# Performance work log

Hardware: AMD Instinct MI355X
Metric: run time of the kernel (lower is better)

Reference implementation:

```python
import math
import jax, jax.numpy as jnp
import numpy as np

NUM_HEADS = 8
ATTN_STD = np.array([1.0, 2.0, 4.0, 8.0, 1.0, 2.0, 4.0, 8.0], dtype=np.float32)
ATTN_OFFSET = np.array([-1.0, -2.0, -4.0, -8.0, -1.0, -2.0, -4.0, -8.0], dtype=np.float32)


def setup_inputs() -> dict:
    key = jax.random.key(0)
    k1, k2, k3 = jax.random.split(key, 3)
    B, L, D = 2, 2048, 1024
    values = jax.random.normal(k1, (B, L, D), dtype=jnp.float32)
    # learned params (init_std = 0.02, matching nn.init.normal_)
    input_weights = 0.02 * jax.random.normal(k2, (D, D), dtype=jnp.float32)
    output_weight = 0.02 * jax.random.normal(k3, (D, D), dtype=jnp.float32)
    return {"values": values, "input_weights": input_weights, "output_weight": output_weight}


def _gaussian_attn_weights(qlen, dtype):
    # Faithful closed form of get_attn_cache retrieval for offsets <= -1:
    # w[h, q, k] = N(k - q - offset_h; std_h), no renormalization, no mask.
    stds = jnp.asarray(ATTN_STD, dtype=dtype)[:, None, None]      # [H,1,1]
    offs = jnp.asarray(ATTN_OFFSET, dtype=dtype)[:, None, None]   # [H,1,1]
    q = jnp.arange(qlen, dtype=dtype)[None, :, None]               # [1,L,1]
    k = jnp.arange(qlen, dtype=dtype)[None, None, :]               # [1,1,L]
    dist = k - q - offs                                            # [H,L,L]
    inv_norm = 1.0 / (stds * math.sqrt(2.0 * math.pi))
    return inv_norm * jnp.exp(-0.5 * (dist / stds) ** 2)           # [H,L,L]


def reference(values, input_weights, output_weight):
    B, L, D = values.shape
    H = NUM_HEADS
    pd = D // H
    # project(): F.linear(values, input_weights) then split into heads
    v = values @ input_weights.T                                   # [B,L,D]
    v = v.reshape(B, L, H, pd).transpose(0, 2, 1, 3)               # [B,H,L,pd]
    probs = _gaussian_attn_weights(L, values.dtype)                # [H,L,L]
    attended = jnp.einsum('hqk,bhkd->bhqd', probs, v)              # [B,H,L,pd]
    attended = attended.transpose(0, 2, 1, 3).reshape(B, L, D)     # merge heads
    # output_projection (Linear, no bias)
    return attended @ output_weight.T
```

## Files before the change

kernel.cpp:

```cpp
#include <hip/hip_runtime.h>
#include <hip/hip_bf16.h>

#define L_SEQ   2048
#define D_MODEL 1024
#define B_SZ    2
#define LP      (L_SEQ + 192)
#define PADF    96

typedef __attribute__((ext_vector_type(8))) short bf16x8;
typedef __attribute__((ext_vector_type(4))) float f32x4;

__device__ __forceinline__ void gll16(const void* g, void* l) {
    __builtin_amdgcn_global_load_lds(
        (const __attribute__((address_space(1))) unsigned int*)(g),
        (__attribute__((address_space(3))) unsigned int*)(l),
        16, 0, 0);
}

__device__ __forceinline__ ushort bf16_hi(float x) {
    __hip_bfloat16 h = __float2bfloat16(x);
    return *reinterpret_cast<ushort*>(&h);
}
__device__ __forceinline__ float bf16_back(ushort u) {
    __hip_bfloat16 h = *reinterpret_cast<__hip_bfloat16*>(&u);
    return __bfloat162float(h);
}

__global__ __launch_bounds__(256) void prep(const float* __restrict__ values,
                                            const float* __restrict__ w_in,
                                            const float* __restrict__ w_out,
                                            ushort* __restrict__ Ph, ushort* __restrict__ Pl,
                                            ushort* __restrict__ Wh, ushort* __restrict__ Wl,
                                            ushort* __restrict__ W2h, ushort* __restrict__ W2l,
                                            float* __restrict__ vpad)
{
    int blk = blockIdx.x;
    if (blk < 384) {
        const int r  = blk / 96;
        const int rr = blk % 96;
        const int b  = r >> 1;
        const int row0 = (r & 1) ? (LP - 96) : 0;
        size_t off = ((size_t)b * LP + row0 + rr) * D_MODEL + threadIdx.x * 4;
        *(float4*)(vpad + off) = make_float4(0.f, 0.f, 0.f, 0.f);
        return;
    }
    blk -= 384;
    const float* src;
    ushort *oh, *ol;
    if (blk < 4096)      { src = values; oh = Ph;  ol = Pl;  }
    else if (blk < 5120) { src = w_in;   oh = Wh;  ol = Wl;  blk -= 4096; }
    else                 { src = w_out;  oh = W2h; ol = W2l; blk -= 5120; }

    const size_t i = ((size_t)blk * 256 + threadIdx.x) * 4;
    float4 v = *(const float4*)(src + i);
    float f[4] = {v.x, v.y, v.z, v.w};
    ushort hb[4], lb[4];
    #pragma unroll
    for (int j = 0; j < 4; ++j) {
        hb[j] = bf16_hi(f[j]);
        lb[j] = bf16_hi(f[j] - bf16_back(hb[j]));
    }
    *(ushort4*)(oh + i) = make_ushort4(hb[0], hb[1], hb[2], hb[3]);
    *(ushort4*)(ol + i) = make_ushort4(lb[0], lb[1], lb[2], lb[3]);
}

template<int DO_PAD>
__global__ __launch_bounds__(512) void gemm_split(const ushort* __restrict__ Ah,
                                                  const ushort* __restrict__ Al,
                                                  const ushort* __restrict__ Bh,
                                                  const ushort* __restrict__ Bl,
                                                  float* __restrict__ C)
{
    __shared__ __align__(16) ushort lds[4][4][128 * 32];

    const int tid = threadIdx.x;
    const int w   = tid >> 6;
    const int l   = tid & 63;

    const int bn  = (blockIdx.x & 7) * 128;
    const int bm  = (blockIdx.x >> 3) * 128;

    const int srow   = tid >> 2;
    const int schunk = (tid & 3) ^ ((tid >> 3) & 3);
    const ushort* gAh = Ah + (size_t)(bm + srow) * 1024 + schunk * 8;
    const ushort* gAl = Al + (size_t)(bm + srow) * 1024 + schunk * 8;
    const ushort* gBh = Bh + (size_t)(bn + srow) * 1024 + schunk * 8;
    const ushort* gBl = Bl + (size_t)(bn + srow) * 1024 + schunk * 8;
    const int ldst = tid * 8;

    const int fr  = l & 15;
    const int fq  = l >> 4;
    const int swz = (fr >> 1) & 3;
    const int rdo = (fq ^ swz) << 3;
    const int wr  = w >> 2;
    const int wc  = w & 3;

    f32x4 acc[4][2];
    #pragma unroll
    for (int mi = 0; mi < 4; ++mi)
        #pragma unroll
        for (int ni = 0; ni < 2; ++ni) acc[mi][ni] = (f32x4){0.f, 0.f, 0.f, 0.f};

    #define STAGE(buf, kt)                                        \
        do {                                                      \
            const size_t ko_ = (size_t)(kt) * 32;                 \
            gll16(gAh + ko_, &lds[(buf)][0][ldst]);               \
            gll16(gAl + ko_, &lds[(buf)][1][ldst]);               \
            gll16(gBh + ko_, &lds[(buf)][2][ldst]);               \
            gll16(gBl + ko_, &lds[(buf)][3][ldst]);               \
        } while (0)

    #define WAITBAR(N) asm volatile("s_waitcnt vmcnt(" #N ")\n\ts_barrier" ::: "memory")

    #define COMPUTE(cur)                                                                   \
        do {                                                                               \
            bf16x8 ah[4], al[4];                                                           \
            _Pragma("unroll")                                                              \
            for (int mi = 0; mi < 4; ++mi) {                                               \
                const int row = wr * 64 + mi * 16 + fr;                                    \
                ah[mi] = *(const bf16x8*)&lds[(cur)][0][row * 32 + rdo];                   \
                al[mi] = *(const bf16x8*)&lds[(cur)][1][row * 32 + rdo];                   \
            }                                                                              \
            _Pragma("unroll")                                                              \
            for (int ni = 0; ni < 2; ++ni) {                                               \
                const int row = wc * 32 + ni * 16 + fr;                                    \
                bf16x8 bh = *(const bf16x8*)&lds[(cur)][2][row * 32 + rdo];                \
                bf16x8 bl = *(const bf16x8*)&lds[(cur)][3][row * 32 + rdo];                \
                _Pragma("unroll")                                                          \
                for (int mi = 0; mi < 4; ++mi)                                             \
                    acc[mi][ni] = __builtin_amdgcn_mfma_f32_16x16x32_bf16(ah[mi], bh, acc[mi][ni], 0, 0, 0); \
                _Pragma("unroll")                                                          \
                for (int mi = 0; mi < 4; ++mi)                                             \
                    acc[mi][ni] = __builtin_amdgcn_mfma_f32_16x16x32_bf16(al[mi], bh, acc[mi][ni], 0, 0, 0); \
                _Pragma("unroll")                                                          \
                for (int mi = 0; mi < 4; ++mi)                                             \
                    acc[mi][ni] = __builtin_amdgcn_mfma_f32_16x16x32_bf16(ah[mi], bl, acc[mi][ni], 0, 0, 0); \
            }                                                                              \
        } while (0)

    STAGE(0, 0);
    STAGE(1, 1);
    STAGE(2, 2);

    for (int kt = 0; kt < 29; ++kt) {
        WAITBAR(8);
        STAGE((kt + 3) & 3, kt + 3);
        COMPUTE(kt & 3);
    }
    WAITBAR(8); COMPUTE(1);
    WAITBAR(4); COMPUTE(2);
    WAITBAR(0); COMPUTE(3);

    #undef STAGE
    #undef WAITBAR
    #undef COMPUTE

    #pragma unroll
    for (int mi = 0; mi < 4; ++mi) {
        #pragma unroll
        for (int ni = 0; ni < 2; ++ni) {
            const int col = bn + wc * 32 + ni * 16 + fr;
            #pragma unroll
            for (int j = 0; j < 4; ++j) {
                const int m = bm + wr * 64 + mi * 16 + fq * 4 + j;
                const size_t row = DO_PAD ? ((size_t)(m >> 11) * LP + (m & (L_SEQ - 1)) + PADF)
                                          : (size_t)m;
                C[row * 1024 + col] = acc[mi][ni][j];
            }
        }
    }
}

__global__ __launch_bounds__(256) void gauss_conv_split(const float* __restrict__ vpad,
                                                        ushort* __restrict__ Oh,
                                                        ushort* __restrict__ Ol)
{
    __shared__ __align__(16) float xs[256 * 64];
    __shared__ float wt[128];

    const int tid = threadIdx.x;
    const int d0  = blockIdx.x * 64;
    const int q0  = blockIdx.y * 128;
    const int b   = blockIdx.z;
    const int h   = blockIdx.x >> 1;

    if (tid < 128) {
        const float sig = (float)(1 << (h & 3));
        const float t = ((float)(tid - 71) + sig) / sig;
        wt[tid] = (0.39894228040143267794f / sig) * expf(-0.5f * t * t);
    }

    const float* src = vpad + ((size_t)b * LP + (PADF - 71) + q0) * 1024 + d0;
    #pragma unroll
    for (int p = 0; p < 16; ++p) {
        const int f   = p * 256 + tid;
        const int row = f >> 4;
        const int c4  = (f & 15) * 4;
        gll16(src + (size_t)row * 1024 + c4, &xs[f * 4]);
    }
    __syncthreads();

    const int d     = tid & 63;
    const int qbase = (tid >> 6) * 32;

    float acc[32];
    #pragma unroll
    for (int qq = 0; qq < 32; ++qq) acc[qq] = 0.f;

    #pragma unroll 1
    for (int c = 0; c < 8; ++c) {
        float xw[47];
        const float* xp = &xs[(qbase + c * 16) * 64 + d];
        #pragma unroll
        for (int j = 0; j < 47; ++j) xw[j] = xp[j * 64];
        #pragma unroll
        for (int dd = 0; dd < 16; ++dd) {
            const float wv = wt[c * 16 + dd];
            #pragma unroll
            for (int qq = 0; qq < 32; ++qq)
                acc[qq] = fmaf(wv, xw[dd + qq], acc[qq]);
        }
    }

    ushort* oh = Oh + ((size_t)b * L_SEQ + q0 + qbase) * 1024 + d0 + d;
    ushort* ol = Ol + ((size_t)b * L_SEQ + q0 + qbase) * 1024 + d0 + d;
    #pragma unroll
    for (int qq = 0; qq < 32; ++qq) {
        const ushort hv = bf16_hi(acc[qq]);
        oh[(size_t)qq * 1024] = hv;
        ol[(size_t)qq * 1024] = bf16_hi(acc[qq] - bf16_back(hv));
    }
}

extern "C" void kernel_launch(void* const* d_in, const int* in_sizes, int n_in,
                              void* d_out, int out_size, void* d_ws, size_t ws_size,
                              hipStream_t stream)
{
    const float* values = (const float*)d_in[0];
    const float* w_in   = (const float*)d_in[1];
    const float* w_out  = (const float*)d_in[2];
    float* out = (float*)d_out;

    float*  vpad = (float*)d_ws;
    ushort* Ph  = (ushort*)(vpad + (size_t)B_SZ * LP * D_MODEL);
    ushort* Pl  = Ph  + (size_t)4096 * 1024;
    ushort* Wh  = Pl  + (size_t)4096 * 1024;
    ushort* Wl  = Wh  + (size_t)1024 * 1024;
    ushort* W2h = Wl  + (size_t)1024 * 1024;
    ushort* W2l = W2h + (size_t)1024 * 1024;

    prep<<<dim3(384 + 4096 + 1024 + 1024), dim3(256), 0, stream>>>(
        values, w_in, w_out, Ph, Pl, Wh, Wl, W2h, W2l, vpad);

    gemm_split<1><<<dim3(256), dim3(512), 0, stream>>>(Ph, Pl, Wh, Wl, vpad);

    dim3 cgrid(D_MODEL / 64, L_SEQ / 128, B_SZ);
    gauss_conv_split<<<cgrid, dim3(256), 0, stream>>>(vpad, Ph, Pl);

    gemm_split<0><<<dim3(256), dim3(512), 0, stream>>>(Ph, Pl, W2h, W2l, out);
}
```

Before: 151.2 us.

## Split GEMM into 128x64 tiles with 256 threads, triple-buffered LDS, XCD-aware mapping

The split-bf16 GEMM now uses 128x64 output tiles computed by 4 waves, so 512 blocks launch instead of 256 and two blocks can share a CU. The LDS pipeline drops from four stages to three, which shrinks shared memory per block. Block-to-tile mapping places adjacent N tiles on the same XCD so they reuse A rows in cache. In exchange, each block reloads its A tile for only half the N width, which raises total global traffic.

```diff
diff --git a/kernel.cpp b/kernel.cpp
--- a/kernel.cpp
+++ b/kernel.cpp
@@ -65,35 +65,39 @@
 }
 
 template<int DO_PAD>
-__global__ __launch_bounds__(512) void gemm_split(const ushort* __restrict__ Ah,
-                                                  const ushort* __restrict__ Al,
-                                                  const ushort* __restrict__ Bh,
-                                                  const ushort* __restrict__ Bl,
-                                                  float* __restrict__ C)
-{
-    __shared__ __align__(16) ushort lds[4][4][128 * 32];
+__global__ __launch_bounds__(256, 2) void gemm_split(const ushort* __restrict__ Ah,
+                                                     const ushort* __restrict__ Al,
+                                                     const ushort* __restrict__ Bh,
+                                                     const ushort* __restrict__ Bl,
+                                                     float* __restrict__ C)
+{
+    __shared__ __align__(16) ushort lds[3][12288];
 
     const int tid = threadIdx.x;
     const int w   = tid >> 6;
     const int l   = tid & 63;
 
-    const int bn  = (blockIdx.x & 7) * 128;
-    const int bm  = (blockIdx.x >> 3) * 128;
+    const int xcd = blockIdx.x & 7;
+    const int p   = blockIdx.x >> 3;
+    const int bn  = (xcd * 2 + (p & 1)) * 64;
+    const int bm  = (p >> 1) * 128;
 
     const int srow   = tid >> 2;
     const int schunk = (tid & 3) ^ ((tid >> 3) & 3);
-    const ushort* gAh = Ah + (size_t)(bm + srow) * 1024 + schunk * 8;
-    const ushort* gAl = Al + (size_t)(bm + srow) * 1024 + schunk * 8;
-    const ushort* gBh = Bh + (size_t)(bn + srow) * 1024 + schunk * 8;
-    const ushort* gBl = Bl + (size_t)(bn + srow) * 1024 + schunk * 8;
+    const ushort* gAh0 = Ah + (size_t)(bm + srow) * 1024 + schunk * 8;
+    const ushort* gAh1 = gAh0 + (size_t)64 * 1024;
+    const ushort* gAl0 = Al + (size_t)(bm + srow) * 1024 + schunk * 8;
+    const ushort* gAl1 = gAl0 + (size_t)64 * 1024;
+    const ushort* gBh  = Bh + (size_t)(bn + srow) * 1024 + schunk * 8;
+    const ushort* gBl  = Bl + (size_t)(bn + srow) * 1024 + schunk * 8;
     const int ldst = tid * 8;
 
     const int fr  = l & 15;
     const int fq  = l >> 4;
     const int swz = (fr >> 1) & 3;
     const int rdo = (fq ^ swz) << 3;
-    const int wr  = w >> 2;
-    const int wc  = w & 3;
+    const int wr  = w >> 1;
+    const int wc  = w & 1;
 
     f32x4 acc[4][2];
     #pragma unroll
@@ -104,10 +108,12 @@
     #define STAGE(buf, kt)                                        \
         do {                                                      \
             const size_t ko_ = (size_t)(kt) * 32;                 \
-            gll16(gAh + ko_, &lds[(buf)][0][ldst]);               \
-            gll16(gAl + ko_, &lds[(buf)][1][ldst]);               \
-            gll16(gBh + ko_, &lds[(buf)][2][ldst]);               \
-            gll16(gBl + ko_, &lds[(buf)][3][ldst]);               \
+            gll16(gAh0 + ko_, &lds[(buf)][ldst]);                 \
+            gll16(gAh1 + ko_, &lds[(buf)][2048 + ldst]);          \
+            gll16(gAl0 + ko_, &lds[(buf)][4096 + ldst]);          \
+            gll16(gAl1 + ko_, &lds[(buf)][6144 + ldst]);          \
+            gll16(gBh  + ko_, &lds[(buf)][8192 + ldst]);          \
+            gll16(gBl  + ko_, &lds[(buf)][10240 + ldst]);         \
         } while (0)
 
     #define WAITBAR(N) asm volatile("s_waitcnt vmcnt(" #N ")\n\ts_barrier" ::: "memory")
@@ -118,14 +124,14 @@
             _Pragma("unroll")                                                              \
             for (int mi = 0; mi < 4; ++mi) {                                               \
                 const int row = wr * 64 + mi * 16 + fr;                                    \
-                ah[mi] = *(const bf16x8*)&lds[(cur)][0][row * 32 + rdo];                   \
-                al[mi] = *(const bf16x8*)&lds[(cur)][1][row * 32 + rdo];                   \
+                ah[mi] = *(const bf16x8*)&lds[(cur)][row * 32 + rdo];                      \
+                al[mi] = *(const bf16x8*)&lds[(cur)][4096 + row * 32 + rdo];               \
             }                                                                              \
             _Pragma("unroll")                                                              \
             for (int ni = 0; ni < 2; ++ni) {                                               \
                 const int row = wc * 32 + ni * 16 + fr;                                    \
-                bf16x8 bh = *(const bf16x8*)&lds[(cur)][2][row * 32 + rdo];                \
-                bf16x8 bl = *(const bf16x8*)&lds[(cur)][3][row * 32 + rdo];                \
+                bf16x8 bh = *(const bf16x8*)&lds[(cur)][8192 + row * 32 + rdo];            \
+                bf16x8 bl = *(const bf16x8*)&lds[(cur)][10240 + row * 32 + rdo];           \
                 _Pragma("unroll")                                                          \
                 for (int mi = 0; mi < 4; ++mi)                                             \
                     acc[mi][ni] = __builtin_amdgcn_mfma_f32_16x16x32_bf16(ah[mi], bh, acc[mi][ni], 0, 0, 0); \
@@ -140,16 +146,14 @@
 
     STAGE(0, 0);
     STAGE(1, 1);
-    STAGE(2, 2);
-
-    for (int kt = 0; kt < 29; ++kt) {
-        WAITBAR(8);
-        STAGE((kt + 3) & 3, kt + 3);
-        COMPUTE(kt & 3);
-    }
-    WAITBAR(8); COMPUTE(1);
-    WAITBAR(4); COMPUTE(2);
-    WAITBAR(0); COMPUTE(3);
+
+    for (int kt = 0; kt < 30; kt += 3) {
+        WAITBAR(6); STAGE(2, kt + 2); COMPUTE(0);
+        WAITBAR(6); STAGE(0, kt + 3); COMPUTE(1);
+        WAITBAR(6); STAGE(1, kt + 4); COMPUTE(2);
+    }
+    WAITBAR(6); COMPUTE(0);
+    WAITBAR(0); COMPUTE(1);
 
     #undef STAGE
     #undef WAITBAR
@@ -252,10 +256,10 @@
     prep<<<dim3(384 + 4096 + 1024 + 1024), dim3(256), 0, stream>>>(
         values, w_in, w_out, Ph, Pl, Wh, Wl, W2h, W2l, vpad);
 
-    gemm_split<1><<<dim3(256), dim3(512), 0, stream>>>(Ph, Pl, Wh, Wl, vpad);
+    gemm_split<1><<<dim3(512), dim3(256), 0, stream>>>(Ph, Pl, Wh, Wl, vpad);
 
     dim3 cgrid(D_MODEL / 64, L_SEQ / 128, B_SZ);
     gauss_conv_split<<<cgrid, dim3(256), 0, stream>>>(vpad, Ph, Pl);
 
-    gemm_split<0><<<dim3(256), dim3(512), 0, stream>>>(Ph, Pl, W2h, W2l, out);
-}
+    gemm_split<0><<<dim3(512), dim3(256), 0, stream>>>(Ph, Pl, W2h, W2l, out);
+}
```

Measured after the change: 157.4 us. +4.1%, slower.

## Fuse prep, two GEMMs and Gaussian conv into one persistent kernel with grid barriers

Applied to the files above, without the earlier changes.

Replaces four separate kernel launches with a single persistent 256-block kernel that runs prep, the input GEMM, the Gaussian convolution and the output GEMM as phases separated by atomic-counter grid barriers. The counter lives in the last padded row of vpad, so the zero-fill skips that row. The conv phase is reshaped to 512 threads with a 128-column tile so it matches the GEMM block shape, and LDS is shared between phases through a union. This removes launch gaps and tail effects between kernels. In exchange it relies on all 256 blocks being co-resident, adds spin-wait barrier cost, and gives prep and conv less parallelism than they had before.

```diff
diff --git a/kernel.cpp b/kernel.cpp
--- a/kernel.cpp
+++ b/kernel.cpp
@@ -26,53 +26,79 @@
     return __bfloat162float(h);
 }
 
-__global__ __launch_bounds__(256) void prep(const float* __restrict__ values,
-                                            const float* __restrict__ w_in,
-                                            const float* __restrict__ w_out,
-                                            ushort* __restrict__ Ph, ushort* __restrict__ Pl,
-                                            ushort* __restrict__ Wh, ushort* __restrict__ Wl,
-                                            ushort* __restrict__ W2h, ushort* __restrict__ W2l,
-                                            float* __restrict__ vpad)
-{
-    int blk = blockIdx.x;
-    if (blk < 384) {
-        const int r  = blk / 96;
-        const int rr = blk % 96;
-        const int b  = r >> 1;
-        const int row0 = (r & 1) ? (LP - 96) : 0;
-        size_t off = ((size_t)b * LP + row0 + rr) * D_MODEL + threadIdx.x * 4;
-        *(float4*)(vpad + off) = make_float4(0.f, 0.f, 0.f, 0.f);
-        return;
-    }
-    blk -= 384;
-    const float* src;
-    ushort *oh, *ol;
-    if (blk < 4096)      { src = values; oh = Ph;  ol = Pl;  }
-    else if (blk < 5120) { src = w_in;   oh = Wh;  ol = Wl;  blk -= 4096; }
-    else                 { src = w_out;  oh = W2h; ol = W2l; blk -= 5120; }
-
-    const size_t i = ((size_t)blk * 256 + threadIdx.x) * 4;
-    float4 v = *(const float4*)(src + i);
-    float f[4] = {v.x, v.y, v.z, v.w};
-    ushort hb[4], lb[4];
-    #pragma unroll
-    for (int j = 0; j < 4; ++j) {
-        hb[j] = bf16_hi(f[j]);
-        lb[j] = bf16_hi(f[j] - bf16_back(hb[j]));
-    }
-    *(ushort4*)(oh + i) = make_ushort4(hb[0], hb[1], hb[2], hb[3]);
-    *(ushort4*)(ol + i) = make_ushort4(lb[0], lb[1], lb[2], lb[3]);
+__global__ __launch_bounds__(64) void init_ctr(int* __restrict__ ctr)
+{
+    if (threadIdx.x < 16) ctr[threadIdx.x] = 0;
+}
+
+__device__ __forceinline__ void grid_barrier(int* ctr, int target)
+{
+    __syncthreads();
+    if (threadIdx.x == 0) {
+        __threadfence();
+        __hip_atomic_fetch_add(ctr, 1, __ATOMIC_ACQ_REL, __HIP_MEMORY_SCOPE_AGENT);
+        int guard = 0;
+        while (__hip_atomic_load(ctr, __ATOMIC_ACQUIRE, __HIP_MEMORY_SCOPE_AGENT) < target
+               && guard < (1 << 22)) {
+            __builtin_amdgcn_s_sleep(16);
+            ++guard;
+        }
+    }
+    __syncthreads();
+}
+
+__device__ __forceinline__ void phase_prep(const float* __restrict__ values,
+                                           const float* __restrict__ w_in,
+                                           const float* __restrict__ w_out,
+                                           ushort* __restrict__ Ph, ushort* __restrict__ Pl,
+                                           ushort* __restrict__ Wh, ushort* __restrict__ Wl,
+                                           ushort* __restrict__ W2h, ushort* __restrict__ W2l,
+                                           float* __restrict__ vpad)
+{
+    const int NZ = 98304;
+    const int NV = 1048576;
+    const int NW = 262144;
+    const int TOT = NZ + NV + 2 * NW;
+    for (int u = blockIdx.x * 512 + threadIdx.x; u < TOT; u += 256 * 512) {
+        if (u < NZ) {
+            const int r  = u / 24576;
+            const int rr = (u - r * 24576) >> 8;
+            const int c4 = u & 255;
+            if (r == 3 && rr == 95) continue;
+            const int b = r >> 1;
+            const int row0 = (r & 1) ? (LP - 96) : 0;
+            *(float4*)(vpad + (size_t)(b * LP + row0 + rr) * 1024 + c4 * 4) =
+                make_float4(0.f, 0.f, 0.f, 0.f);
+            continue;
+        }
+        int v = u - NZ;
+        const float* src;
+        ushort *oh, *ol;
+        if (v < NV)           { src = values; oh = Ph;  ol = Pl;  }
+        else if (v < NV + NW) { src = w_in;   oh = Wh;  ol = Wl;  v -= NV; }
+        else                  { src = w_out;  oh = W2h; ol = W2l; v -= NV + NW; }
+        const size_t i = (size_t)v * 4;
+        float4 x = *(const float4*)(src + i);
+        float f[4] = {x.x, x.y, x.z, x.w};
+        ushort hb[4], lb[4];
+        #pragma unroll
+        for (int j = 0; j < 4; ++j) {
+            hb[j] = bf16_hi(f[j]);
+            lb[j] = bf16_hi(f[j] - bf16_back(hb[j]));
+        }
+        *(ushort4*)(oh + i) = make_ushort4(hb[0], hb[1], hb[2], hb[3]);
+        *(ushort4*)(ol + i) = make_ushort4(lb[0], lb[1], lb[2], lb[3]);
+    }
 }
 
 template<int DO_PAD>
-__global__ __launch_bounds__(512) void gemm_split(const ushort* __restrict__ Ah,
-                                                  const ushort* __restrict__ Al,
-                                                  const ushort* __restrict__ Bh,
-                                                  const ushort* __restrict__ Bl,
-                                                  float* __restrict__ C)
-{
-    __shared__ __align__(16) ushort lds[4][4][128 * 32];
-
+__device__ __forceinline__ void phase_gemm(ushort lds[4][4][4096],
+                                           const ushort* __restrict__ Ah,
+                                           const ushort* __restrict__ Al,
+                                           const ushort* __restrict__ Bh,
+                                           const ushort* __restrict__ Bl,
+                                           float* __restrict__ C)
+{
     const int tid = threadIdx.x;
     const int w   = tid >> 6;
     const int l   = tid & 63;
@@ -171,18 +197,18 @@
     }
 }
 
-__global__ __launch_bounds__(256) void gauss_conv_split(const float* __restrict__ vpad,
-                                                        ushort* __restrict__ Oh,
-                                                        ushort* __restrict__ Ol)
-{
-    __shared__ __align__(16) float xs[256 * 64];
-    __shared__ float wt[128];
-
+__device__ __forceinline__ void phase_conv(float* xs ,
+                                           float* wt ,
+                                           const float* __restrict__ vpad,
+                                           ushort* __restrict__ Oh,
+                                           ushort* __restrict__ Ol)
+{
     const int tid = threadIdx.x;
-    const int d0  = blockIdx.x * 64;
-    const int q0  = blockIdx.y * 128;
-    const int b   = blockIdx.z;
-    const int h   = blockIdx.x >> 1;
+    const int blk = blockIdx.x;
+    const int d0  = (blk & 7) * 128;
+    const int q0  = ((blk >> 3) & 15) * 128;
+    const int b   = blk >> 7;
+    const int h   = blk & 7;
 
     if (tid < 128) {
         const float sig = (float)(1 << (h & 3));
@@ -193,15 +219,15 @@
     const float* src = vpad + ((size_t)b * LP + (PADF - 71) + q0) * 1024 + d0;
     #pragma unroll
     for (int p = 0; p < 16; ++p) {
-        const int f   = p * 256 + tid;
-        const int row = f >> 4;
-        const int c4  = (f & 15) * 4;
-        gll16(src + (size_t)row * 1024 + c4, &xs[f * 4]);
+        const int f   = p * 512 + tid;
+        const int row = f >> 5;
+        const int c4  = (f & 31) * 4;
+        gll16(src + (size_t)row * 1024 + c4, xs + (size_t)f * 4);
     }
     __syncthreads();
 
-    const int d     = tid & 63;
-    const int qbase = (tid >> 6) * 32;
+    const int d     = tid & 127;
+    const int qbase = (tid >> 7) * 32;
 
     float acc[32];
     #pragma unroll
@@ -210,9 +236,9 @@
     #pragma unroll 1
     for (int c = 0; c < 8; ++c) {
         float xw[47];
-        const float* xp = &xs[(qbase + c * 16) * 64 + d];
-        #pragma unroll
-        for (int j = 0; j < 47; ++j) xw[j] = xp[j * 64];
+        const float* xp = xs + (qbase + c * 16) * 128 + d;
+        #pragma unroll
+        for (int j = 0; j < 47; ++j) xw[j] = xp[j * 128];
         #pragma unroll
         for (int dd = 0; dd < 16; ++dd) {
             const float wv = wt[c * 16 + dd];
@@ -230,6 +256,32 @@
         oh[(size_t)qq * 1024] = hv;
         ol[(size_t)qq * 1024] = bf16_hi(acc[qq] - bf16_back(hv));
     }
+}
+
+__global__ __launch_bounds__(512, 1) void mega(const float* __restrict__ values,
+                                               const float* __restrict__ w_in,
+                                               const float* __restrict__ w_out,
+                                               float* __restrict__ out,
+                                               float* __restrict__ vpad,
+                                               ushort* __restrict__ Ph, ushort* __restrict__ Pl,
+                                               ushort* __restrict__ Wh, ushort* __restrict__ Wl,
+                                               ushort* __restrict__ W2h, ushort* __restrict__ W2l,
+                                               int* __restrict__ ctr)
+{
+    union SharedU {
+        ushort g[4][4][4096];
+        float  xs[256 * 128];
+    };
+    __shared__ SharedU sh;
+    __shared__ float wt[128];
+
+    phase_prep(values, w_in, w_out, Ph, Pl, Wh, Wl, W2h, W2l, vpad);
+    grid_barrier(ctr, 256);
+    phase_gemm<1>(sh.g, Ph, Pl, Wh, Wl, vpad);
+    grid_barrier(ctr, 512);
+    phase_conv(sh.xs, wt, vpad, Ph, Pl);
+    grid_barrier(ctr, 768);
+    phase_gemm<0>(sh.g, Ph, Pl, W2h, W2l, out);
 }
 
 extern "C" void kernel_launch(void* const* d_in, const int* in_sizes, int n_in,
@@ -248,14 +300,9 @@
     ushort* Wl  = Wh  + (size_t)1024 * 1024;
     ushort* W2h = Wl  + (size_t)1024 * 1024;
     ushort* W2l = W2h + (size_t)1024 * 1024;
-
-    prep<<<dim3(384 + 4096 + 1024 + 1024), dim3(256), 0, stream>>>(
-        values, w_in, w_out, Ph, Pl, Wh, Wl, W2h, W2l, vpad);
-
-    gemm_split<1><<<dim3(256), dim3(512), 0, stream>>>(Ph, Pl, Wh, Wl, vpad);
-
-    dim3 cgrid(D_MODEL / 64, L_SEQ / 128, B_SZ);
-    gauss_conv_split<<<cgrid, dim3(256), 0, stream>>>(vpad, Ph, Pl);
-
-    gemm_split<0><<<dim3(256), dim3(512), 0, stream>>>(Ph, Pl, W2h, W2l, out);
-}
+    int* ctr = (int*)(vpad + (size_t)(2 * LP - 1) * 1024);
+
+    init_ctr<<<dim3(1), dim3(64), 0, stream>>>(ctr);
+    mega<<<dim3(256), dim3(512), 0, stream>>>(values, w_in, w_out, out,
+                                              vpad, Ph, Pl, Wh, Wl, W2h, W2l, ctr);
+}
```

Result: slower. 251.1 us (+66.1%).

## Interleave global-to-LDS prefetch with MFMA phases using barriers and setprio

Applied to the files above, without the earlier changes.

Splits each k-step of the split-bf16 GEMM into two half-phases. Each phase issues part of the next stage's global_load_lds, then runs its MFMA cluster under raised wave priority, with barriers between phases. The aim is to spread memory issue across the compute and keep waves in lockstep so MFMA and load traffic overlap better. It adds four extra barriers per k-step, which could cost more than the overlap gains.

```diff
diff --git a/kernel.cpp b/kernel.cpp
--- a/kernel.cpp
+++ b/kernel.cpp
@@ -71,7 +71,7 @@
                                                   const ushort* __restrict__ Bl,
                                                   float* __restrict__ C)
 {
-    __shared__ __align__(16) ushort lds[4][4][128 * 32];
+    __shared__ __align__(16) ushort lds[4][4][4096];
 
     const int tid = threadIdx.x;
     const int w   = tid >> 6;
@@ -111,8 +111,9 @@
         } while (0)
 
     #define WAITBAR(N) asm volatile("s_waitcnt vmcnt(" #N ")\n\ts_barrier" ::: "memory")
-
-    #define COMPUTE(cur)                                                                   \
+    #define BAR() __builtin_amdgcn_s_barrier()
+
+    #define STEP(cur, DO_STG, kt3)                                                         \
         do {                                                                               \
             bf16x8 ah[4], al[4];                                                           \
             _Pragma("unroll")                                                              \
@@ -121,21 +122,48 @@
                 ah[mi] = *(const bf16x8*)&lds[(cur)][0][row * 32 + rdo];                   \
                 al[mi] = *(const bf16x8*)&lds[(cur)][1][row * 32 + rdo];                   \
             }                                                                              \
-            _Pragma("unroll")                                                              \
-            for (int ni = 0; ni < 2; ++ni) {                                               \
-                const int row = wc * 32 + ni * 16 + fr;                                    \
-                bf16x8 bh = *(const bf16x8*)&lds[(cur)][2][row * 32 + rdo];                \
-                bf16x8 bl = *(const bf16x8*)&lds[(cur)][3][row * 32 + rdo];                \
-                _Pragma("unroll")                                                          \
-                for (int mi = 0; mi < 4; ++mi)                                             \
-                    acc[mi][ni] = __builtin_amdgcn_mfma_f32_16x16x32_bf16(ah[mi], bh, acc[mi][ni], 0, 0, 0); \
-                _Pragma("unroll")                                                          \
-                for (int mi = 0; mi < 4; ++mi)                                             \
-                    acc[mi][ni] = __builtin_amdgcn_mfma_f32_16x16x32_bf16(al[mi], bh, acc[mi][ni], 0, 0, 0); \
-                _Pragma("unroll")                                                          \
-                for (int mi = 0; mi < 4; ++mi)                                             \
-                    acc[mi][ni] = __builtin_amdgcn_mfma_f32_16x16x32_bf16(ah[mi], bl, acc[mi][ni], 0, 0, 0); \
+            const int rowb0 = wc * 32 + fr;                                                \
+            bf16x8 bh0 = *(const bf16x8*)&lds[(cur)][2][rowb0 * 32 + rdo];                 \
+            bf16x8 bl0 = *(const bf16x8*)&lds[(cur)][3][rowb0 * 32 + rdo];                 \
+            if (DO_STG) {                                                                  \
+                const size_t ko_ = (size_t)(kt3) * 32;                                     \
+                gll16(gAh + ko_, &lds[((cur) + 3) & 3][0][ldst]);                          \
+                gll16(gAl + ko_, &lds[((cur) + 3) & 3][1][ldst]);                          \
             }                                                                              \
+            BAR();                                                                         \
+            __builtin_amdgcn_s_setprio(1);                                                 \
+            _Pragma("unroll")                                                              \
+            for (int mi = 0; mi < 4; ++mi)                                                 \
+                acc[mi][0] = __builtin_amdgcn_mfma_f32_16x16x32_bf16(ah[mi], bh0, acc[mi][0], 0, 0, 0); \
+            _Pragma("unroll")                                                              \
+            for (int mi = 0; mi < 4; ++mi)                                                 \
+                acc[mi][0] = __builtin_amdgcn_mfma_f32_16x16x32_bf16(al[mi], bh0, acc[mi][0], 0, 0, 0); \
+            _Pragma("unroll")                                                              \
+            for (int mi = 0; mi < 4; ++mi)                                                 \
+                acc[mi][0] = __builtin_amdgcn_mfma_f32_16x16x32_bf16(ah[mi], bl0, acc[mi][0], 0, 0, 0); \
+            __builtin_amdgcn_s_setprio(0);                                                 \
+            BAR();                                                                         \
+            const int rowb1 = wc * 32 + 16 + fr;                                           \
+            bf16x8 bh1 = *(const bf16x8*)&lds[(cur)][2][rowb1 * 32 + rdo];                 \
+            bf16x8 bl1 = *(const bf16x8*)&lds[(cur)][3][rowb1 * 32 + rdo];                 \
+            if (DO_STG) {                                                                  \
+                const size_t ko_ = (size_t)(kt3) * 32;                                     \
+                gll16(gBh + ko_, &lds[((cur) + 3) & 3][2][ldst]);                          \
+                gll16(gBl + ko_, &lds[((cur) + 3) & 3][3][ldst]);                          \
+            }                                                                              \
+            BAR();                                                                         \
+            __builtin_amdgcn_s_setprio(1);                                                 \
+            _Pragma("unroll")                                                              \
+            for (int mi = 0; mi < 4; ++mi)                                                 \
+                acc[mi][1] = __builtin_amdgcn_mfma_f32_16x16x32_bf16(ah[mi], bh1, acc[mi][1], 0, 0, 0); \
+            _Pragma("unroll")                                                              \
+            for (int mi = 0; mi < 4; ++mi)                                                 \
+                acc[mi][1] = __builtin_amdgcn_mfma_f32_16x16x32_bf16(al[mi], bh1, acc[mi][1], 0, 0, 0); \
+            _Pragma("unroll")                                                              \
+            for (int mi = 0; mi < 4; ++mi)                                                 \
+                acc[mi][1] = __builtin_amdgcn_mfma_f32_16x16x32_bf16(ah[mi], bl1, acc[mi][1], 0, 0, 0); \
+            __builtin_amdgcn_s_setprio(0);                                                 \
+            BAR();                                                                         \
         } while (0)
 
     STAGE(0, 0);
@@ -144,16 +172,16 @@
 
     for (int kt = 0; kt < 29; ++kt) {
         WAITBAR(8);
-        STAGE((kt + 3) & 3, kt + 3);
-        COMPUTE(kt & 3);
-    }
-    WAITBAR(8); COMPUTE(1);
-    WAITBAR(4); COMPUTE(2);
-    WAITBAR(0); COMPUTE(3);
+        STEP(kt & 3, 1, kt + 3);
+    }
+    WAITBAR(8); STEP(1, 0, 0);
+    WAITBAR(4); STEP(2, 0, 0);
+    WAITBAR(0); STEP(3, 0, 0);
 
     #undef STAGE
     #undef WAITBAR
-    #undef COMPUTE
+    #undef BAR
+    #undef STEP
 
     #pragma unroll
     for (int mi = 0; mi < 4; ++mi) {
```

New measurement: 160.1 us. +5.8%, slower.
